# Optimization experiments

Hardware: AMD Instinct MI355X
Metric: run time of the kernel (lower is better)

Reference implementation:

```python
import jax, jax.numpy as jnp
import numpy as np

EPS = 1e-5

def setup_inputs() -> dict:
    key = jax.random.key(0)
    ks = jax.random.split(key, 5)
    B, L, D = 8, 2048, 1024
    scale = 0.02
    return {
        "x": jax.random.normal(ks[0], (B, L, D), dtype=jnp.float32),
        "Wk": jax.random.normal(ks[1], (D, D), dtype=jnp.float32) * scale,
        "Wkg": jax.random.normal(ks[2], (D, D), dtype=jnp.float32) * scale,
        "bkg": jnp.zeros((D,), dtype=jnp.float32),
        "Wout": jax.random.normal(ks[3], (D, D), dtype=jnp.float32) * scale,
        "num_heads": 16,
    }

def reference(x, Wk, Wkg, bkg, Wout, num_heads):
    B, L, D = x.shape
    n = num_heads
    d = D // n  # per-head dim
    k = x @ Wk.T                                   # [B, L, D]
    g = jax.nn.sigmoid(x @ Wkg.T + bkg)            # [B, L, D]
    # [B, L, n, d] -> scan over L
    k = k.reshape(B, L, n, d).transpose(1, 0, 2, 3)  # [L, B, n, d]
    g = g.reshape(B, L, n, d).transpose(1, 0, 2, 3)
    inv_sqrt_d = 1.0 / np.sqrt(d)

    def step(h, xs):
        x_t, g_t = xs
        rms = jnp.sqrt(jnp.sum(h * h, axis=-1, keepdims=True)) * inv_sqrt_d
        h_hat = h / (rms + EPS)
        h_new = h_hat * g_t + x_t
        return h_new, h_new

    h0 = jnp.zeros((B, n, d), dtype=x.dtype)
    _, o = jax.lax.scan(step, h0, (k, g))          # [L, B, n, d]
    o = o.transpose(1, 0, 2, 3).reshape(B, L, D)   # [B, L, D]
    return o @ Wout.T
```

## Files before the change

kernel.cpp:

```cpp
#include <hip/hip_runtime.h>
#include <hip/hip_bf16.h>
#include <math.h>

#define BATCH 8
#define SEQL  2048
#define DIM   1024
#define MROWS (BATCH * SEQL)

typedef _Float16 f16;
typedef _Float16 f16x8 __attribute__((ext_vector_type(8)));
typedef _Float16 f16x4 __attribute__((ext_vector_type(4)));
typedef _Float16 f16x2 __attribute__((ext_vector_type(2)));
typedef float f32x4 __attribute__((ext_vector_type(4)));

typedef const __attribute__((address_space(1))) void* gp_t;
typedef __attribute__((address_space(3))) void* lp_t;
#define GLL(src, dst) __builtin_amdgcn_global_load_lds((gp_t)(src), (lp_t)(dst), 16, 0, 0)

__global__ __launch_bounds__(256) void cvt_all(const float* __restrict__ x,
                                               const float* __restrict__ Wk,
                                               const float* __restrict__ Wkg,
                                               const float* __restrict__ Wout,
                                               f16* __restrict__ xh,
                                               f16* __restrict__ Wcat,
                                               f16* __restrict__ Wouth)
{
    int i = blockIdx.x * 256 + threadIdx.x;
    const float* src; f16* dst;
    if (i < 2097152)      { src = x;    dst = xh;             }
    else if (i < 2228224) { src = Wk;   dst = Wcat;           i -= 2097152; }
    else if (i < 2359296) { src = Wkg;  dst = Wcat + 1048576; i -= 2228224; }
    else                  { src = Wout; dst = Wouth;          i -= 2359296; }
    const float4* p = (const float4*)src + (size_t)i * 2;
    const float4 a = p[0], b = p[1];
    f16x8 v;
    v[0] = (f16)a.x; v[1] = (f16)a.y; v[2] = (f16)a.z; v[3] = (f16)a.w;
    v[4] = (f16)b.x; v[5] = (f16)b.y; v[6] = (f16)b.z; v[7] = (f16)b.w;
    *(f16x8*)(dst + (size_t)i * 8) = v;
}

template<int MODE>
__global__ __launch_bounds__(512, 2) void gemm8(const f16* __restrict__ A,
                                                const f16* __restrict__ Bw,
                                                const float* __restrict__ bias,
                                                void* __restrict__ C0,
                                                void* __restrict__ C1)
{
    constexpr int K   = 1024;
    constexpr int NTI = MODE ? 8 : 4;
    constexpr int NKT = 16;
    __shared__ f16 lds[2][2][256 * 64];

    const int tid = threadIdx.x;
    const int w = tid >> 6, l = tid & 63;
    const int wm = w >> 2, wn = w & 3;
    const int lrow = l & 15;
    const int l7 = l & 7, lk = l >> 4;

    const int cpx = gridDim.x >> 3;
    const int lt  = (blockIdx.x & 7) * cpx + (blockIdx.x >> 3);
    const int bm  = (lt / NTI) * 256;
    const int bn  = (lt % NTI) * 256;

    const int srl   = tid >> 3;
    const int sg    = tid & 7;
    const int scolx = (sg ^ (srl & 7)) * 8;

    const int g0 = ((lk) ^ l7) * 8;
    const int g1 = ((4 + lk) ^ l7) * 8;

#define STAGE(t, m, P, rowbase, h)                                                       \
    do {                                                                                 \
        const int _rf0 = (h) * 128 + srl;                                                \
        GLL((P) + (size_t)((rowbase) + _rf0) * K + (t) * 64 + scolx,                     \
            &lds[(t) & 1][m][_rf0 * 64 + sg * 8]);                                       \
        const int _rf1 = _rf0 + 64;                                                      \
        GLL((P) + (size_t)((rowbase) + _rf1) * K + (t) * 64 + scolx,                     \
            &lds[(t) & 1][m][_rf1 * 64 + sg * 8]);                                       \
    } while (0)

    f32x4 acc[8][4];
    #pragma unroll
    for (int mi = 0; mi < 8; ++mi)
        #pragma unroll
        for (int ni = 0; ni < 4; ++ni) acc[mi][ni] = (f32x4){0.f, 0.f, 0.f, 0.f};

    f16x8 bf[4][2];

#define PHASE(p, cur, STG, LOAD_B)                                                       \
    do {                                                                                 \
        const f16* _ab = &lds[cur][0][0];                                                \
        const int _ar = (wm * 128 + (2 * (p)) * 16 + lrow) * 64;                         \
        f16x8 a00 = *(const f16x8*)(_ab + _ar + g0);                                     \
        f16x8 a01 = *(const f16x8*)(_ab + _ar + g1);                                     \
        f16x8 a10 = *(const f16x8*)(_ab + _ar + 1024 + g0);                              \
        f16x8 a11 = *(const f16x8*)(_ab + _ar + 1024 + g1);                              \
        if (LOAD_B) {                                                                    \
            const f16* _bb = &lds[cur][1][0];                                            \
            _Pragma("unroll")                                                            \
            for (int ni = 0; ni < 4; ++ni) {                                             \
                const int _br = (wn * 64 + ni * 16 + lrow) * 64;                         \
                bf[ni][0] = *(const f16x8*)(_bb + _br + g0);                             \
                bf[ni][1] = *(const f16x8*)(_bb + _br + g1);                             \
            }                                                                            \
        }                                                                                \
        STG;                                                                             \
        __builtin_amdgcn_s_barrier();                                                    \
        asm volatile("s_waitcnt lgkmcnt(0)" ::: "memory");                               \
        __builtin_amdgcn_sched_barrier(0);                                               \
        __builtin_amdgcn_s_setprio(1);                                                   \
        _Pragma("unroll")                                                                \
        for (int ni = 0; ni < 4; ++ni) {                                                 \
            acc[2*(p)][ni]   = __builtin_amdgcn_mfma_f32_16x16x32_f16(a00, bf[ni][0], acc[2*(p)][ni], 0, 0, 0);   \
            acc[2*(p)][ni]   = __builtin_amdgcn_mfma_f32_16x16x32_f16(a01, bf[ni][1], acc[2*(p)][ni], 0, 0, 0);   \
            acc[2*(p)+1][ni] = __builtin_amdgcn_mfma_f32_16x16x32_f16(a10, bf[ni][0], acc[2*(p)+1][ni], 0, 0, 0); \
            acc[2*(p)+1][ni] = __builtin_amdgcn_mfma_f32_16x16x32_f16(a11, bf[ni][1], acc[2*(p)+1][ni], 0, 0, 0); \
        }                                                                                \
        __builtin_amdgcn_s_setprio(0);                                                   \
    } while (0)

    STAGE(0, 0, A, bm, 0);  STAGE(0, 0, A, bm, 1);
    STAGE(0, 1, Bw, bn, 0); STAGE(0, 1, Bw, bn, 1);
    STAGE(1, 1, Bw, bn, 0); STAGE(1, 1, Bw, bn, 1);
    asm volatile("s_waitcnt vmcnt(4)" ::: "memory");
    __builtin_amdgcn_s_barrier();

    for (int t = 0; t < NKT; ++t) {
        const int cur = t & 1;
        PHASE(0, cur, { if (t + 1 < NKT) STAGE(t + 1, 0, A, bm, 0); }, 1);
        __builtin_amdgcn_s_barrier();
        PHASE(1, cur, { if (t + 1 < NKT) STAGE(t + 1, 0, A, bm, 1); }, 0);
        __builtin_amdgcn_s_barrier();
        PHASE(2, cur, { if (t + 2 < NKT) STAGE(t + 2, 1, Bw, bn, 0); }, 0);
        __builtin_amdgcn_s_barrier();
        PHASE(3, cur, { if (t + 2 < NKT) STAGE(t + 2, 1, Bw, bn, 1); }, 0);
        if (t + 2 < NKT)      asm volatile("s_waitcnt vmcnt(4)" ::: "memory");
        else if (t + 1 < NKT) asm volatile("s_waitcnt vmcnt(0)" ::: "memory");
        __builtin_amdgcn_s_barrier();
    }
#undef PHASE
#undef STAGE

    const int orow = (l >> 4) * 4;
    const int ocol = l & 15;
    #pragma unroll
    for (int mi = 0; mi < 8; ++mi) {
        #pragma unroll
        for (int ni = 0; ni < 4; ++ni) {
            const int col  = bn + wn * 64 + ni * 16 + ocol;
            const int row0 = bm + wm * 128 + mi * 16 + orow;
            #pragma unroll
            for (int r = 0; r < 4; ++r) {
                float v = acc[mi][ni][r];
                if (MODE == 0) {
                    ((float*)C0)[(size_t)(row0 + r) * DIM + col] = v;
                } else {
                    if (col < DIM) {
                        ((f16*)C0)[(size_t)(row0 + r) * DIM + col] = (f16)v;
                    } else {
                        v += bias[col - DIM];
                        v = 1.f / (1.f + __expf(-v));
                        ((f16*)C1)[(size_t)(row0 + r) * DIM + (col - DIM)] = (f16)v;
                    }
                }
            }
        }
    }
}

template<int CTRL>
__device__ __forceinline__ float dpp_add_f(float s) {
    int t = __builtin_amdgcn_update_dpp(0, __float_as_int(s), CTRL, 0xF, 0xF, true);
    return s + __int_as_float(t);
}

__device__ __forceinline__ float sumsq4(f16x2 a, f16x2 b) {
    return __builtin_amdgcn_fdot2(a, a, __builtin_amdgcn_fdot2(b, b, 0.f, false), false);
}

#define PF 16
#define CHK 128
#define WARM 128

__global__ __launch_bounds__(64) void scan_kernel(const f16* __restrict__ Kv,
                                                  const f16* __restrict__ Gv,
                                                  f16* __restrict__ Ov)
{
    const int w = blockIdx.x & 31;
    const int c = blockIdx.x >> 5;
    const int l = threadIdx.x;

    const int t0   = (c == 0) ? 0 : (c * CHK - WARM);
    const int warm = c * CHK - t0;

    const size_t base = (size_t)(w >> 2) * (SEQL * DIM) + (size_t)((w & 3) * 256 + l * 4);
    size_t off = base + (size_t)t0 * DIM;

    f16x2 h01 = (f16x2){(f16)0.f, (f16)0.f};
    f16x2 h23 = (f16x2){(f16)0.f, (f16)0.f};

    f16x4 kb[PF], gb[PF];
    #pragma unroll
    for (int u = 0; u < PF; ++u) {
        kb[u] = *(const f16x4*)(Kv + off + (size_t)u * DIM);
        gb[u] = *(const f16x4*)(Gv + off + (size_t)u * DIM);
    }

    #define SCAN_STEP(kc, gc, DO_ST)                                                   \
        do {                                                                           \
            const f16x2 k01 = __builtin_shufflevector((kc), (kc), 0, 1);               \
            const f16x2 k23 = __builtin_shufflevector((kc), (kc), 2, 3);               \
            const f16x2 g01 = __builtin_shufflevector((gc), (gc), 0, 1);               \
            const f16x2 g23 = __builtin_shufflevector((gc), (gc), 2, 3);               \
            const f16x2 u01 = h01 * g01;                             \
            const f16x2 u23 = h23 * g23;                                               \
            float s = sumsq4(h01, h23);                                                \
            s = dpp_add_f<0xB1>(s);                                          \
            s = dpp_add_f<0x4E>(s);                                          \
            s = dpp_add_f<0x141>(s);                                         \
            s = dpp_add_f<0x140>(s);                                         \
            const float inv = __builtin_amdgcn_rsqf(fmaf(s, 0.015625f, 1e-8f));        \
            const f16 ih = (f16)inv;                                                   \
            const f16x2 iv = (f16x2){ih, ih};                                          \
            h01 = u01 * iv + k01;                                    \
            h23 = u23 * iv + k23;                                                      \
            if (DO_ST) {                                                               \
                f16x4 o;                                                               \
                o[0] = h01[0]; o[1] = h01[1]; o[2] = h23[0]; o[3] = h23[1];            \
                *(f16x4*)(Ov + off) = o;                                               \
            }                                                                          \
            off += DIM;                                                                \
        } while (0)

    for (int tb = 0; tb < warm; tb += PF) {
        #pragma unroll
        for (int u = 0; u < PF; ++u) {
            const f16x4 kc = kb[u], gc = gb[u];
            const size_t poff = off + (size_t)PF * DIM;
            kb[u] = *(const f16x4*)(Kv + poff);
            gb[u] = *(const f16x4*)(Gv + poff);
            SCAN_STEP(kc, gc, 0);
        }
    }
    for (int tb = 0; tb < CHK - PF; tb += PF) {
        #pragma unroll
        for (int u = 0; u < PF; ++u) {
            const f16x4 kc = kb[u], gc = gb[u];
            const size_t poff = off + (size_t)PF * DIM;
            kb[u] = *(const f16x4*)(Kv + poff);
            gb[u] = *(const f16x4*)(Gv + poff);
            SCAN_STEP(kc, gc, 1);
        }
    }
    #pragma unroll
    for (int u = 0; u < PF; ++u) {
        const f16x4 kc = kb[u], gc = gb[u];
        SCAN_STEP(kc, gc, 1);
    }
    #undef SCAN_STEP
}

extern "C" void kernel_launch(void* const* d_in, const int* in_sizes, int n_in,
                              void* d_out, int out_size, void* d_ws, size_t ws_size,
                              hipStream_t stream) {
    const float* x    = (const float*)d_in[0];
    const float* Wk   = (const float*)d_in[1];
    const float* Wkg  = (const float*)d_in[2];
    const float* bkg  = (const float*)d_in[3];
    const float* Wout = (const float*)d_in[4];
    float* out = (float*)d_out;

    f16* xh    = (f16*)d_ws;
    f16* Kh    = xh    + (size_t)MROWS * DIM;
    f16* Gh    = Kh    + (size_t)MROWS * DIM;
    f16* Wcat  = Gh    + (size_t)MROWS * DIM;
    f16* Wouth = Wcat  + (size_t)2 * DIM * DIM;

    cvt_all<<<dim3(9728), dim3(256), 0, stream>>>(x, Wk, Wkg, Wout, xh, Wcat, Wouth);

    gemm8<1><<<dim3(512), dim3(512), 0, stream>>>(xh, Wcat, bkg, Kh, Gh);
    scan_kernel<<<dim3(512), dim3(64), 0, stream>>>(Kh, Gh, xh);
    gemm8<0><<<dim3(256), dim3(512), 0, stream>>>(xh, Wouth, nullptr, out, nullptr);
}
```

Before: 189.2 us.

## Single-buffer GEMM LDS with fine-grained quarter-tile A staging pipeline

Replaces the double-buffered LDS layout (2x2x256x64 f16) with single A and B buffers. A tiles are now staged in quarter slices interleaved with compute phases, and each phase opens with its own vmcnt wait and barrier. Halving LDS use per block could allow more blocks per CU or leave LDS headroom, and the load pipeline becomes finer grained. The cost is tighter synchronization and a risk of stalls if loads do not arrive in time, since the buffer is overwritten while later phases still need to read it.

```diff
diff --git a/kernel.cpp b/kernel.cpp
--- a/kernel.cpp
+++ b/kernel.cpp
@@ -49,7 +49,8 @@
     constexpr int K   = 1024;
     constexpr int NTI = MODE ? 8 : 4;
     constexpr int NKT = 16;
-    __shared__ f16 lds[2][2][256 * 64];
+    __shared__ f16 ldsA[256 * 64];
+    __shared__ f16 ldsB[256 * 64];
 
     const int tid = threadIdx.x;
     const int w = tid >> 6, l = tid & 63;
@@ -65,20 +66,25 @@
     const int srl   = tid >> 3;
     const int sg    = tid & 7;
     const int scolx = (sg ^ (srl & 7)) * 8;
+    const int aR0 = (srl < 32) ? srl : (96 + srl);
 
     const int g0 = ((lk) ^ l7) * 8;
     const int g1 = ((4 + lk) ^ l7) * 8;
 
-#define STAGE(t, m, P, rowbase, h)                                                       \
+#define STAGE_AQ(tt, p)                                                                  \
     do {                                                                                 \
-        const int _rf0 = (h) * 128 + srl;                                                \
-        GLL((P) + (size_t)((rowbase) + _rf0) * K + (t) * 64 + scolx,                     \
-            &lds[(t) & 1][m][_rf0 * 64 + sg * 8]);                                       \
-        const int _rf1 = _rf0 + 64;                                                      \
-        GLL((P) + (size_t)((rowbase) + _rf1) * K + (t) * 64 + scolx,                     \
-            &lds[(t) & 1][m][_rf1 * 64 + sg * 8]);                                       \
+        const int _R = 32 * (p) + aR0;                                                   \
+        GLL(A + (size_t)(bm + _R) * K + (tt) * 64 + scolx, ldsA + _R * 64 + sg * 8);     \
     } while (0)
 
+#define STAGE_BH(tt, h)                                                                  \
+    do {                                                                                 \
+        const int _r0 = (h) * 128 + srl;                                                 \
+        GLL(Bw + (size_t)(bn + _r0) * K + (tt) * 64 + scolx, ldsB + _r0 * 64 + sg * 8);  \
+        const int _r1 = _r0 + 64;                                                        \
+        GLL(Bw + (size_t)(bn + _r1) * K + (tt) * 64 + scolx, ldsB + _r1 * 64 + sg * 8);  \
+    } while (0)
+
     f32x4 acc[8][4];
     #pragma unroll
     for (int mi = 0; mi < 8; ++mi)
@@ -87,25 +93,24 @@
 
     f16x8 bf[4][2];
 
-#define PHASE(p, cur, STG, LOAD_B)                                                       \
+#define PHASE(p, VK, STG)                                                                \
     do {                                                                                 \
-        const f16* _ab = &lds[cur][0][0];                                                \
-        const int _ar = (wm * 128 + (2 * (p)) * 16 + lrow) * 64;                         \
-        f16x8 a00 = *(const f16x8*)(_ab + _ar + g0);                                     \
-        f16x8 a01 = *(const f16x8*)(_ab + _ar + g1);                                     \
-        f16x8 a10 = *(const f16x8*)(_ab + _ar + 1024 + g0);                              \
-        f16x8 a11 = *(const f16x8*)(_ab + _ar + 1024 + g1);                              \
-        if (LOAD_B) {                                                                    \
-            const f16* _bb = &lds[cur][1][0];                                            \
+        asm volatile("s_waitcnt vmcnt(" #VK ")" ::: "memory");                           \
+        __builtin_amdgcn_s_barrier();                                                    \
+        const int _ar = (wm * 128 + 32 * (p) + lrow) * 64;                               \
+        f16x8 a00 = *(const f16x8*)(ldsA + _ar + g0);                                    \
+        f16x8 a01 = *(const f16x8*)(ldsA + _ar + g1);                                    \
+        f16x8 a10 = *(const f16x8*)(ldsA + _ar + 1024 + g0);                             \
+        f16x8 a11 = *(const f16x8*)(ldsA + _ar + 1024 + g1);                             \
+        if ((p) == 0) {                                                                  \
             _Pragma("unroll")                                                            \
             for (int ni = 0; ni < 4; ++ni) {                                             \
                 const int _br = (wn * 64 + ni * 16 + lrow) * 64;                         \
-                bf[ni][0] = *(const f16x8*)(_bb + _br + g0);                             \
-                bf[ni][1] = *(const f16x8*)(_bb + _br + g1);                             \
+                bf[ni][0] = *(const f16x8*)(ldsB + _br + g0);                            \
+                bf[ni][1] = *(const f16x8*)(ldsB + _br + g1);                            \
             }                                                                            \
         }                                                                                \
         STG;                                                                             \
-        __builtin_amdgcn_s_barrier();                                                    \
         asm volatile("s_waitcnt lgkmcnt(0)" ::: "memory");                               \
         __builtin_amdgcn_sched_barrier(0);                                               \
         __builtin_amdgcn_s_setprio(1);                                                   \
@@ -119,27 +124,23 @@
         __builtin_amdgcn_s_setprio(0);                                                   \
     } while (0)
 
-    STAGE(0, 0, A, bm, 0);  STAGE(0, 0, A, bm, 1);
-    STAGE(0, 1, Bw, bn, 0); STAGE(0, 1, Bw, bn, 1);
-    STAGE(1, 1, Bw, bn, 0); STAGE(1, 1, Bw, bn, 1);
-    asm volatile("s_waitcnt vmcnt(4)" ::: "memory");
-    __builtin_amdgcn_s_barrier();
-
-    for (int t = 0; t < NKT; ++t) {
-        const int cur = t & 1;
-        PHASE(0, cur, { if (t + 1 < NKT) STAGE(t + 1, 0, A, bm, 0); }, 1);
-        __builtin_amdgcn_s_barrier();
-        PHASE(1, cur, { if (t + 1 < NKT) STAGE(t + 1, 0, A, bm, 1); }, 0);
-        __builtin_amdgcn_s_barrier();
-        PHASE(2, cur, { if (t + 2 < NKT) STAGE(t + 2, 1, Bw, bn, 0); }, 0);
-        __builtin_amdgcn_s_barrier();
-        PHASE(3, cur, { if (t + 2 < NKT) STAGE(t + 2, 1, Bw, bn, 1); }, 0);
-        if (t + 2 < NKT)      asm volatile("s_waitcnt vmcnt(4)" ::: "memory");
-        else if (t + 1 < NKT) asm volatile("s_waitcnt vmcnt(0)" ::: "memory");
-        __builtin_amdgcn_s_barrier();
-    }
+    STAGE_BH(0, 0); STAGE_AQ(0, 0);
+    STAGE_BH(0, 1); STAGE_AQ(0, 1);
+    STAGE_AQ(0, 2);
+
+    for (int t = 0; t < NKT - 1; ++t) {
+        PHASE(0, 2, { STAGE_AQ(t, 3); });
+        PHASE(1, 2, { STAGE_BH(t + 1, 0); STAGE_AQ(t + 1, 0); });
+        PHASE(2, 4, { STAGE_BH(t + 1, 1); STAGE_AQ(t + 1, 1); });
+        PHASE(3, 6, { STAGE_AQ(t + 1, 2); });
+    }
+    PHASE(0, 2, { STAGE_AQ(NKT - 1, 3); });
+    PHASE(1, 2, {});
+    PHASE(2, 1, {});
+    PHASE(3, 0, {});
 #undef PHASE
-#undef STAGE
+#undef STAGE_AQ
+#undef STAGE_BH
 
     const int orow = (l >> 4) * 4;
     const int ocol = l & 15;
@@ -212,17 +213,17 @@
             const f16x2 k23 = __builtin_shufflevector((kc), (kc), 2, 3);               \
             const f16x2 g01 = __builtin_shufflevector((gc), (gc), 0, 1);               \
             const f16x2 g23 = __builtin_shufflevector((gc), (gc), 2, 3);               \
-            const f16x2 u01 = h01 * g01;                             \
+            const f16x2 u01 = h01 * g01;                                               \
             const f16x2 u23 = h23 * g23;                                               \
             float s = sumsq4(h01, h23);                                                \
-            s = dpp_add_f<0xB1>(s);                                          \
-            s = dpp_add_f<0x4E>(s);                                          \
-            s = dpp_add_f<0x141>(s);                                         \
-            s = dpp_add_f<0x140>(s);                                         \
+            s = dpp_add_f<0xB1>(s);                                                    \
+            s = dpp_add_f<0x4E>(s);                                                    \
+            s = dpp_add_f<0x141>(s);                                                   \
+            s = dpp_add_f<0x140>(s);                                                   \
             const float inv = __builtin_amdgcn_rsqf(fmaf(s, 0.015625f, 1e-8f));        \
             const f16 ih = (f16)inv;                                                   \
             const f16x2 iv = (f16x2){ih, ih};                                          \
-            h01 = u01 * iv + k01;                                    \
+            h01 = u01 * iv + k01;                                                      \
             h23 = u23 * iv + k23;                                                      \
             if (DO_ST) {                                                               \
                 f16x4 o;                                                               \
```

New measurement: 186.0 us. About the same (-1.7%).
